# Kernel optimization log

Measured on AMD Instinct MI355X. Metric: run time of the kernel, lower is better.

Reference implementation:

```python
import jax, jax.numpy as jnp
import numpy as np

B, N, M = 64, 1024, 1024
MAX_ITER = 10      # init default max_iter
EPS = 1e-4         # init default epsilon


def setup_inputs() -> dict:
    key = jax.random.key(0)
    k1, k2, k3 = jax.random.split(key, 3)
    s = jax.random.uniform(k1, (B, N, M), dtype=jnp.float32)
    # ragged valid sizes per batch element, in [N//2, N]
    nrows = jax.random.randint(k2, (B,), N // 2, N + 1, dtype=jnp.int32)
    ncols = jax.random.randint(k3, (B,), M // 2, M + 1, dtype=jnp.int32)
    return {"s": s, "nrows": nrows, "ncols": ncols}


def reference(s, nrows, ncols):
    # Faithful vectorized form of the torch loop:
    #   even iter: sum[b,i,j] = sum_{k<nrows[b]} s[b,k,j]  (masked column sums)
    #   odd  iter: sum[b,i,j] = sum_{k<ncols[b]} s[b,i,k]  (masked row sums)
    #   then s[b,i,j] *= 1/sum inside the [nrows[b], ncols[b]] block, 0 outside.
    Bb, Nn, Mm = s.shape
    row_mask = jnp.arange(Nn)[None, :] < nrows[:, None]          # [B, N]
    col_mask = jnp.arange(Mm)[None, :] < ncols[:, None]          # [B, M]
    block = row_mask[:, :, None] & col_mask[:, None, :]          # [B, N, M]

    s = s + jnp.float32(EPS)
    for i in range(MAX_ITER):
        if i % 2 == 0:
            # column normalization: sum over valid rows
            d = jnp.sum(jnp.where(row_mask[:, :, None], s, 0.0), axis=1, keepdims=True)  # [B,1,M]
            d = jnp.where(col_mask[:, None, :], d, 1.0)  # safe denom outside block
        else:
            # row normalization: sum over valid cols
            d = jnp.sum(jnp.where(col_mask[:, None, :], s, 0.0), axis=2, keepdims=True)  # [B,N,1]
            d = jnp.where(row_mask[:, :, None], d, 1.0)
        s = jnp.where(block, s / d, 0.0)
    return s
```

## Files before the change

kernel.cpp:

```cpp
#include <hip/hip_runtime.h>


#define BB 64
#define NN 1024
#define MM 1024
#define EPS 1e-4f

typedef _Float16 half_t;
typedef __attribute__((ext_vector_type(4))) _Float16 half4_t;
typedef __attribute__((ext_vector_type(8))) _Float16 half8_t;
typedef __attribute__((ext_vector_type(4))) float float4_t;

__global__ __launch_bounds__(256) void prep_kernel(
    const float* __restrict__ s, const int* __restrict__ nrows,
    const int* __restrict__ ncols, half_t* __restrict__ H,
    float* __restrict__ P) {
  int b = blockIdx.z, rc = blockIdx.y, stripe = blockIdx.x;
  int nr = nrows[b], nc = ncols[b];
  float* Pp = P + ((size_t)rc * BB + b) * MM + stripe * 128;
  if (stripe * 128 >= nc) {
    if (threadIdx.x < 128) Pp[threadIdx.x] = 0.f;
    return;
  }
  int tc = threadIdx.x & 31, tr = threadIdx.x >> 5;
  int j0 = stripe * 128 + tc * 4;
  const float* sp = s + (size_t)b * NN * MM + j0;
  half_t* hp = H + (size_t)b * NN * MM + j0;
  float4_t acc = {0.f, 0.f, 0.f, 0.f};
  int base = rc * 128;
#pragma unroll
  for (int it = 0; it < 16; it++) {
    int i = base + it * 8 + tr;
    if (i < nr) {
      float4_t v = *(const float4_t*)(sp + (size_t)i * MM);
      v.x += EPS; v.y += EPS; v.z += EPS; v.w += EPS;
      half4_t h = {(half_t)v.x, (half_t)v.y, (half_t)v.z, (half_t)v.w};
      *(half4_t*)(hp + (size_t)i * MM) = h;
      acc.x += v.x; acc.y += v.y; acc.z += v.z; acc.w += v.w;
    }
  }
  __shared__ float lds[8][128];
  *(float4_t*)&lds[tr][tc * 4] = acc;
  __syncthreads();
  if (threadIdx.x < 128) {
    float s0 = 0.f;
#pragma unroll
    for (int k = 0; k < 8; k++) s0 += lds[k][threadIdx.x];
    Pp[threadIdx.x] = s0;
  }
}

__global__ __launch_bounds__(256) void creduce_kernel(
    const float* __restrict__ P, const int* __restrict__ ncols,
    float* __restrict__ C) {
  int b = blockIdx.y;
  int j = blockIdx.x * 256 + threadIdx.x;
  int nc = ncols[b];
  float s0 = 0.f;
#pragma unroll
  for (int k = 0; k < 8; k++) s0 += P[((size_t)k * BB + b) * MM + j];
  C[b * MM + j] = (j < nc) ? 1.f / s0 : 0.f;
}

__global__ __launch_bounds__(256) void row_kernel(
    const half_t* __restrict__ H, const int* __restrict__ nrows,
    const int* __restrict__ ncols, const float* __restrict__ C,
    float* __restrict__ R) {
  int b = blockIdx.y;
  int nr = nrows[b], nc = ncols[b];
  int w = threadIdx.x >> 6, l = threadIdx.x & 63;
  int i = blockIdx.x * 4 + w;
  if (i >= nr) return;
  const half_t* hp = H + ((size_t)b * NN + i) * MM;
  const float* Cp = C + b * MM;
  float acc = 0.f;
#pragma unroll
  for (int ch = 0; ch < 2; ch++) {
    int base = ch * 512 + l * 8;
    if (base < nc) {
      half8_t h = *(const half8_t*)(hp + base);
      float4_t c0 = *(const float4_t*)(Cp + base);
      float4_t c1 = *(const float4_t*)(Cp + base + 4);
      acc += (float)h[0] * c0.x + (float)h[1] * c0.y + (float)h[2] * c0.z +
             (float)h[3] * c0.w + (float)h[4] * c1.x + (float)h[5] * c1.y +
             (float)h[6] * c1.z + (float)h[7] * c1.w;
    }
  }
#pragma unroll
  for (int off = 32; off > 0; off >>= 1) acc += __shfl_xor(acc, off, 64);
  if (l == 0) R[b * NN + i] = 1.f / acc;
}

__global__ __launch_bounds__(256) void col_kernel(
    const half_t* __restrict__ H, const int* __restrict__ nrows,
    const int* __restrict__ ncols, const float* __restrict__ R,
    float* __restrict__ P) {
  int b = blockIdx.z, rc = blockIdx.y, stripe = blockIdx.x;
  int nr = nrows[b], nc = ncols[b];
  float* Pp = P + ((size_t)rc * BB + b) * MM + stripe * 256;
  if (stripe * 256 >= nc) {
    Pp[threadIdx.x] = 0.f;
    return;
  }
  int tc = threadIdx.x & 31, tr = threadIdx.x >> 5;
  int j0 = stripe * 256 + tc * 8;
  const half_t* hp = H + (size_t)b * NN * MM + j0;
  const float* Rp = R + b * NN;
  float acc[8] = {0.f, 0.f, 0.f, 0.f, 0.f, 0.f, 0.f, 0.f};
  int base = rc * 128;
#pragma unroll
  for (int it = 0; it < 16; it++) {
    int i = base + it * 8 + tr;
    if (i < nr) {
      half8_t h = *(const half8_t*)(hp + (size_t)i * MM);
      float r = Rp[i];
#pragma unroll
      for (int k = 0; k < 8; k++) acc[k] += (float)h[k] * r;
    }
  }
  __shared__ float lds[8][256];
#pragma unroll
  for (int k = 0; k < 8; k++) lds[tr][tc * 8 + k] = acc[k];
  __syncthreads();
  float s0 = 0.f;
#pragma unroll
  for (int k = 0; k < 8; k++) s0 += lds[k][threadIdx.x];
  Pp[threadIdx.x] = s0;
}

__global__ __launch_bounds__(256) void final_kernel(
    const float* __restrict__ s, const int* __restrict__ nrows,
    const int* __restrict__ ncols, const float* __restrict__ C,
    float* __restrict__ out) {
  int b = blockIdx.y;
  int nr = nrows[b], nc = ncols[b];
  int w = threadIdx.x >> 6, l = threadIdx.x & 63;
  int i = blockIdx.x * 4 + w;
  float* op = out + ((size_t)b * NN + i) * MM;
  float4_t z = {0.f, 0.f, 0.f, 0.f};
  if (i >= nr) {
#pragma unroll
    for (int ch = 0; ch < 4; ch++) *(float4_t*)(op + ch * 256 + l * 4) = z;
    return;
  }
  const float* sp = s + ((size_t)b * NN + i) * MM;
  const float* Cp = C + b * MM;
  float4_t sv[4], cv[4];
  float acc = 0.f;
  int nch = (nc + 255) >> 8;
#pragma unroll
  for (int ch = 0; ch < 4; ch++) {
    if (ch < nch) {
      float4_t v = *(const float4_t*)(sp + ch * 256 + l * 4);
      v.x += EPS; v.y += EPS; v.z += EPS; v.w += EPS;
      sv[ch] = v;
      float4_t c = *(const float4_t*)(Cp + ch * 256 + l * 4);
      cv[ch] = c;
      acc += v.x * c.x + v.y * c.y + v.z * c.z + v.w * c.w;
    }
  }
#pragma unroll
  for (int off = 32; off > 0; off >>= 1) acc += __shfl_xor(acc, off, 64);
  float r = 1.f / acc;
#pragma unroll
  for (int ch = 0; ch < 4; ch++) {
    if (ch < nch) {
      float4_t o;
      o.x = sv[ch].x * cv[ch].x * r;
      o.y = sv[ch].y * cv[ch].y * r;
      o.z = sv[ch].z * cv[ch].z * r;
      o.w = sv[ch].w * cv[ch].w * r;
      *(float4_t*)(op + ch * 256 + l * 4) = o;
    } else {
      *(float4_t*)(op + ch * 256 + l * 4) = z;
    }
  }
}

extern "C" void kernel_launch(void* const* d_in, const int* in_sizes, int n_in,
                              void* d_out, int out_size, void* d_ws,
                              size_t ws_size, hipStream_t stream) {
  const float* s = (const float*)d_in[0];
  const int* nrows = (const int*)d_in[1];
  const int* ncols = (const int*)d_in[2];
  float* out = (float*)d_out;
  half_t* H = (half_t*)d_out;
  float* R = (float*)d_ws;
  float* C = R + BB * NN;
  float* P = C + BB * MM;

  dim3 pgrid(8, 8, BB);
  dim3 cgrid(4, 8, BB);
  dim3 rgrid(NN / 4, BB);
  dim3 dgrid(4, BB);

  prep_kernel<<<pgrid, 256, 0, stream>>>(s, nrows, ncols, H, P);
  creduce_kernel<<<dgrid, 256, 0, stream>>>(P, ncols, C);
  for (int t = 0; t < 4; t++) {
    row_kernel<<<rgrid, 256, 0, stream>>>(H, nrows, ncols, C, R);
    col_kernel<<<cgrid, 256, 0, stream>>>(H, nrows, ncols, R, P);
    creduce_kernel<<<dgrid, 256, 0, stream>>>(P, ncols, C);
  }
  final_kernel<<<rgrid, 256, 0, stream>>>(s, nrows, ncols, C, out);
}
```

Baseline: 598.5 us.

## Fuse Sinkhorn iterations into one cooperative persistent kernel with fused row/col passes

Replaces the sequence of prep, row, column, reduce and final kernels with one cooperative kernel that uses grid-wide syncs between phases. The row-normalization dot product and the column partial sums now happen in a single pass over each half-precision row, so each iteration reads H once instead of twice and R no longer goes to memory. This removes about fifteen kernel launches and halves the intermediate traffic. In exchange it adds grid.sync costs, limits the grid to resident blocks, and uses a serial per-row loop with a wave reduction on every row.

After: 1.283 ms. 2.14x slower.

```diff
diff --git a/kernel.cpp b/kernel.cpp
--- a/kernel.cpp
+++ b/kernel.cpp
@@ -1,178 +1,190 @@
 #include <hip/hip_runtime.h>
+#include <hip/hip_cooperative_groups.h>
+
+namespace cg = cooperative_groups;
 
 
 #define BB 64
 #define NN 1024
 #define MM 1024
 #define EPS 1e-4f
+#define NCHUNK 16
+#define NITEM (BB * NCHUNK)
 
 typedef _Float16 half_t;
 typedef __attribute__((ext_vector_type(4))) _Float16 half4_t;
-typedef __attribute__((ext_vector_type(8))) _Float16 half8_t;
 typedef __attribute__((ext_vector_type(4))) float float4_t;
 
-__global__ __launch_bounds__(256) void prep_kernel(
+__device__ __forceinline__ float wave_sum(float v) {
+#pragma unroll
+  for (int off = 32; off > 0; off >>= 1) v += __shfl_xor(v, off, 64);
+  return v;
+}
+
+__global__ __launch_bounds__(256, 4) void sinkhorn_coop(
     const float* __restrict__ s, const int* __restrict__ nrows,
     const int* __restrict__ ncols, half_t* __restrict__ H,
-    float* __restrict__ P) {
-  int b = blockIdx.z, rc = blockIdx.y, stripe = blockIdx.x;
-  int nr = nrows[b], nc = ncols[b];
-  float* Pp = P + ((size_t)rc * BB + b) * MM + stripe * 128;
-  if (stripe * 128 >= nc) {
-    if (threadIdx.x < 128) Pp[threadIdx.x] = 0.f;
-    return;
+    float* __restrict__ C, float* __restrict__ P, float* __restrict__ out) {
+  cg::grid_group grid = cg::this_grid();
+  __shared__ float lds[4][MM];
+  const int tid = threadIdx.x;
+  const int w = tid >> 6, l = tid & 63;
+
+  for (int item = blockIdx.x; item < NITEM; item += gridDim.x) {
+    int b = item >> 4, chunk = item & 15;
+    int nr = nrows[b], nc = ncols[b];
+    int rbase = chunk * 64 + w * 16;
+    const float* sp = s + (size_t)b * NN * MM;
+    half_t* hp = H + (size_t)b * NN * MM;
+    float4_t ca[4];
+#pragma unroll
+    for (int c = 0; c < 4; c++) ca[c] = (float4_t){0.f, 0.f, 0.f, 0.f};
+    int nhere = min(nr - rbase, 16);
+    for (int rr = 0; rr < nhere; rr++) {
+      size_t roff = (size_t)(rbase + rr) * MM;
+#pragma unroll
+      for (int c = 0; c < 4; c++) {
+        if (c * 256 < nc) {
+          float4_t v = *(const float4_t*)(sp + roff + c * 256 + l * 4);
+          v.x += EPS; v.y += EPS; v.z += EPS; v.w += EPS;
+          half4_t h = {(half_t)v.x, (half_t)v.y, (half_t)v.z, (half_t)v.w};
+          *(half4_t*)(hp + roff + c * 256 + l * 4) = h;
+          ca[c].x += v.x; ca[c].y += v.y; ca[c].z += v.z; ca[c].w += v.w;
+        }
+      }
+    }
+    __syncthreads();
+#pragma unroll
+    for (int c = 0; c < 4; c++) *(float4_t*)&lds[w][c * 256 + l * 4] = ca[c];
+    __syncthreads();
+    {
+      float4_t a0 = *(float4_t*)&lds[0][tid * 4];
+      float4_t a1 = *(float4_t*)&lds[1][tid * 4];
+      float4_t a2 = *(float4_t*)&lds[2][tid * 4];
+      float4_t a3 = *(float4_t*)&lds[3][tid * 4];
+      float4_t r;
+      r.x = a0.x + a1.x + a2.x + a3.x;
+      r.y = a0.y + a1.y + a2.y + a3.y;
+      r.z = a0.z + a1.z + a2.z + a3.z;
+      r.w = a0.w + a1.w + a2.w + a3.w;
+      *(float4_t*)(P + (size_t)(chunk * BB + b) * MM + tid * 4) = r;
+    }
+    __syncthreads();
   }
-  int tc = threadIdx.x & 31, tr = threadIdx.x >> 5;
-  int j0 = stripe * 128 + tc * 4;
-  const float* sp = s + (size_t)b * NN * MM + j0;
-  half_t* hp = H + (size_t)b * NN * MM + j0;
-  float4_t acc = {0.f, 0.f, 0.f, 0.f};
-  int base = rc * 128;
-#pragma unroll
-  for (int it = 0; it < 16; it++) {
-    int i = base + it * 8 + tr;
-    if (i < nr) {
-      float4_t v = *(const float4_t*)(sp + (size_t)i * MM);
-      v.x += EPS; v.y += EPS; v.z += EPS; v.w += EPS;
-      half4_t h = {(half_t)v.x, (half_t)v.y, (half_t)v.z, (half_t)v.w};
-      *(half4_t*)(hp + (size_t)i * MM) = h;
-      acc.x += v.x; acc.y += v.y; acc.z += v.z; acc.w += v.w;
-    }
+  grid.sync();
+
+  for (int t = 0; t < 5; t++) {
+    for (int idx = blockIdx.x * 256 + tid; idx < BB * MM;
+         idx += gridDim.x * 256) {
+      int b = idx >> 10, j = idx & 1023;
+      float s0 = 0.f;
+#pragma unroll
+      for (int c = 0; c < NCHUNK; c++) s0 += P[(size_t)(c * BB + b) * MM + j];
+      C[idx] = (j < ncols[b]) ? 1.f / s0 : 0.f;
+    }
+    grid.sync();
+    if (t == 4) break;
+
+    for (int item = blockIdx.x; item < NITEM; item += gridDim.x) {
+      int b = item >> 4, chunk = item & 15;
+      int nr = nrows[b], nc = ncols[b];
+      const float* Cb = C + b * MM;
+      float4_t cv[4];
+#pragma unroll
+      for (int c = 0; c < 4; c++)
+        cv[c] = *(const float4_t*)(Cb + c * 256 + l * 4);
+      float4_t ca[4];
+#pragma unroll
+      for (int c = 0; c < 4; c++) ca[c] = (float4_t){0.f, 0.f, 0.f, 0.f};
+      const half_t* hp = H + (size_t)b * NN * MM;
+      int rbase = chunk * 64 + w * 16;
+      int nhere = min(nr - rbase, 16);
+      for (int rr = 0; rr < nhere; rr++) {
+        size_t roff = (size_t)(rbase + rr) * MM;
+        float4_t f[4];
+        float dot = 0.f;
+#pragma unroll
+        for (int c = 0; c < 4; c++) {
+          if (c * 256 < nc) {
+            half4_t h = *(const half4_t*)(hp + roff + c * 256 + l * 4);
+            f[c].x = (float)h[0]; f[c].y = (float)h[1];
+            f[c].z = (float)h[2]; f[c].w = (float)h[3];
+            dot += f[c].x * cv[c].x + f[c].y * cv[c].y + f[c].z * cv[c].z +
+                   f[c].w * cv[c].w;
+          }
+        }
+        float r = 1.f / wave_sum(dot);
+#pragma unroll
+        for (int c = 0; c < 4; c++) {
+          if (c * 256 < nc) {
+            ca[c].x += f[c].x * r; ca[c].y += f[c].y * r;
+            ca[c].z += f[c].z * r; ca[c].w += f[c].w * r;
+          }
+        }
+      }
+      __syncthreads();
+#pragma unroll
+      for (int c = 0; c < 4; c++) *(float4_t*)&lds[w][c * 256 + l * 4] = ca[c];
+      __syncthreads();
+      {
+        float4_t a0 = *(float4_t*)&lds[0][tid * 4];
+        float4_t a1 = *(float4_t*)&lds[1][tid * 4];
+        float4_t a2 = *(float4_t*)&lds[2][tid * 4];
+        float4_t a3 = *(float4_t*)&lds[3][tid * 4];
+        float4_t r;
+        r.x = a0.x + a1.x + a2.x + a3.x;
+        r.y = a0.y + a1.y + a2.y + a3.y;
+        r.z = a0.z + a1.z + a2.z + a3.z;
+        r.w = a0.w + a1.w + a2.w + a3.w;
+        *(float4_t*)(P + (size_t)(chunk * BB + b) * MM + tid * 4) = r;
+      }
+      __syncthreads();
+    }
+    grid.sync();
   }
-  __shared__ float lds[8][128];
-  *(float4_t*)&lds[tr][tc * 4] = acc;
-  __syncthreads();
-  if (threadIdx.x < 128) {
-    float s0 = 0.f;
-#pragma unroll
-    for (int k = 0; k < 8; k++) s0 += lds[k][threadIdx.x];
-    Pp[threadIdx.x] = s0;
-  }
-}
-
-__global__ __launch_bounds__(256) void creduce_kernel(
-    const float* __restrict__ P, const int* __restrict__ ncols,
-    float* __restrict__ C) {
-  int b = blockIdx.y;
-  int j = blockIdx.x * 256 + threadIdx.x;
-  int nc = ncols[b];
-  float s0 = 0.f;
-#pragma unroll
-  for (int k = 0; k < 8; k++) s0 += P[((size_t)k * BB + b) * MM + j];
-  C[b * MM + j] = (j < nc) ? 1.f / s0 : 0.f;
-}
-
-__global__ __launch_bounds__(256) void row_kernel(
-    const half_t* __restrict__ H, const int* __restrict__ nrows,
-    const int* __restrict__ ncols, const float* __restrict__ C,
-    float* __restrict__ R) {
-  int b = blockIdx.y;
-  int nr = nrows[b], nc = ncols[b];
-  int w = threadIdx.x >> 6, l = threadIdx.x & 63;
-  int i = blockIdx.x * 4 + w;
-  if (i >= nr) return;
-  const half_t* hp = H + ((size_t)b * NN + i) * MM;
-  const float* Cp = C + b * MM;
-  float acc = 0.f;
-#pragma unroll
-  for (int ch = 0; ch < 2; ch++) {
-    int base = ch * 512 + l * 8;
-    if (base < nc) {
-      half8_t h = *(const half8_t*)(hp + base);
-      float4_t c0 = *(const float4_t*)(Cp + base);
-      float4_t c1 = *(const float4_t*)(Cp + base + 4);
-      acc += (float)h[0] * c0.x + (float)h[1] * c0.y + (float)h[2] * c0.z +
-             (float)h[3] * c0.w + (float)h[4] * c1.x + (float)h[5] * c1.y +
-             (float)h[6] * c1.z + (float)h[7] * c1.w;
-    }
-  }
-#pragma unroll
-  for (int off = 32; off > 0; off >>= 1) acc += __shfl_xor(acc, off, 64);
-  if (l == 0) R[b * NN + i] = 1.f / acc;
-}
-
-__global__ __launch_bounds__(256) void col_kernel(
-    const half_t* __restrict__ H, const int* __restrict__ nrows,
-    const int* __restrict__ ncols, const float* __restrict__ R,
-    float* __restrict__ P) {
-  int b = blockIdx.z, rc = blockIdx.y, stripe = blockIdx.x;
-  int nr = nrows[b], nc = ncols[b];
-  float* Pp = P + ((size_t)rc * BB + b) * MM + stripe * 256;
-  if (stripe * 256 >= nc) {
-    Pp[threadIdx.x] = 0.f;
-    return;
-  }
-  int tc = threadIdx.x & 31, tr = threadIdx.x >> 5;
-  int j0 = stripe * 256 + tc * 8;
-  const half_t* hp = H + (size_t)b * NN * MM + j0;
-  const float* Rp = R + b * NN;
-  float acc[8] = {0.f, 0.f, 0.f, 0.f, 0.f, 0.f, 0.f, 0.f};
-  int base = rc * 128;
-#pragma unroll
-  for (int it = 0; it < 16; it++) {
-    int i = base + it * 8 + tr;
-    if (i < nr) {
-      half8_t h = *(const half8_t*)(hp + (size_t)i * MM);
-      float r = Rp[i];
-#pragma unroll
-      for (int k = 0; k < 8; k++) acc[k] += (float)h[k] * r;
-    }
-  }
-  __shared__ float lds[8][256];
-#pragma unroll
-  for (int k = 0; k < 8; k++) lds[tr][tc * 8 + k] = acc[k];
-  __syncthreads();
-  float s0 = 0.f;
-#pragma unroll
-  for (int k = 0; k < 8; k++) s0 += lds[k][threadIdx.x];
-  Pp[threadIdx.x] = s0;
-}
-
-__global__ __launch_bounds__(256) void final_kernel(
-    const float* __restrict__ s, const int* __restrict__ nrows,
-    const int* __restrict__ ncols, const float* __restrict__ C,
-    float* __restrict__ out) {
-  int b = blockIdx.y;
-  int nr = nrows[b], nc = ncols[b];
-  int w = threadIdx.x >> 6, l = threadIdx.x & 63;
-  int i = blockIdx.x * 4 + w;
-  float* op = out + ((size_t)b * NN + i) * MM;
-  float4_t z = {0.f, 0.f, 0.f, 0.f};
-  if (i >= nr) {
-#pragma unroll
-    for (int ch = 0; ch < 4; ch++) *(float4_t*)(op + ch * 256 + l * 4) = z;
-    return;
-  }
-  const float* sp = s + ((size_t)b * NN + i) * MM;
-  const float* Cp = C + b * MM;
-  float4_t sv[4], cv[4];
-  float acc = 0.f;
-  int nch = (nc + 255) >> 8;
-#pragma unroll
-  for (int ch = 0; ch < 4; ch++) {
-    if (ch < nch) {
-      float4_t v = *(const float4_t*)(sp + ch * 256 + l * 4);
-      v.x += EPS; v.y += EPS; v.z += EPS; v.w += EPS;
-      sv[ch] = v;
-      float4_t c = *(const float4_t*)(Cp + ch * 256 + l * 4);
-      cv[ch] = c;
-      acc += v.x * c.x + v.y * c.y + v.z * c.z + v.w * c.w;
-    }
-  }
-#pragma unroll
-  for (int off = 32; off > 0; off >>= 1) acc += __shfl_xor(acc, off, 64);
-  float r = 1.f / acc;
-#pragma unroll
-  for (int ch = 0; ch < 4; ch++) {
-    if (ch < nch) {
-      float4_t o;
-      o.x = sv[ch].x * cv[ch].x * r;
-      o.y = sv[ch].y * cv[ch].y * r;
-      o.z = sv[ch].z * cv[ch].z * r;
-      o.w = sv[ch].w * cv[ch].w * r;
-      *(float4_t*)(op + ch * 256 + l * 4) = o;
-    } else {
-      *(float4_t*)(op + ch * 256 + l * 4) = z;
+
+  for (int item = blockIdx.x; item < NITEM; item += gridDim.x) {
+    int b = item >> 4, chunk = item & 15;
+    int nr = nrows[b], nc = ncols[b];
+    const float* Cb = C + b * MM;
+    float4_t cv[4];
+#pragma unroll
+    for (int c = 0; c < 4; c++) cv[c] = *(const float4_t*)(Cb + c * 256 + l * 4);
+    int rbase = chunk * 64 + w * 16;
+    const float* sp = s + (size_t)b * NN * MM;
+    float* op = out + (size_t)b * NN * MM;
+    float4_t z = {0.f, 0.f, 0.f, 0.f};
+    for (int rr = 0; rr < 16; rr++) {
+      int i = rbase + rr;
+      size_t roff = (size_t)i * MM;
+      if (i < nr) {
+        float4_t f[4];
+        float dot = 0.f;
+#pragma unroll
+        for (int c = 0; c < 4; c++) {
+          if (c * 256 < nc) {
+            float4_t v = *(const float4_t*)(sp + roff + c * 256 + l * 4);
+            v.x += EPS; v.y += EPS; v.z += EPS; v.w += EPS;
+            f[c] = v;
+            dot += v.x * cv[c].x + v.y * cv[c].y + v.z * cv[c].z +
+                   v.w * cv[c].w;
+          }
+        }
+        float r = 1.f / wave_sum(dot);
+#pragma unroll
+        for (int c = 0; c < 4; c++) {
+          float4_t o = z;
+          if (c * 256 < nc) {
+            o.x = f[c].x * cv[c].x * r; o.y = f[c].y * cv[c].y * r;
+            o.z = f[c].z * cv[c].z * r; o.w = f[c].w * cv[c].w * r;
+          }
+          *(float4_t*)(op + roff + c * 256 + l * 4) = o;
+        }
+      } else {
+#pragma unroll
+        for (int c = 0; c < 4; c++)
+          *(float4_t*)(op + roff + c * 256 + l * 4) = z;
+      }
     }
   }
 }
@@ -185,21 +197,18 @@
   const int* ncols = (const int*)d_in[2];
   float* out = (float*)d_out;
   half_t* H = (half_t*)d_out;
-  float* R = (float*)d_ws;
-  float* C = R + BB * NN;
+  float* C = (float*)d_ws;
   float* P = C + BB * MM;
 
-  dim3 pgrid(8, 8, BB);
-  dim3 cgrid(4, 8, BB);
-  dim3 rgrid(NN / 4, BB);
-  dim3 dgrid(4, BB);
-
-  prep_kernel<<<pgrid, 256, 0, stream>>>(s, nrows, ncols, H, P);
-  creduce_kernel<<<dgrid, 256, 0, stream>>>(P, ncols, C);
-  for (int t = 0; t < 4; t++) {
-    row_kernel<<<rgrid, 256, 0, stream>>>(H, nrows, ncols, C, R);
-    col_kernel<<<cgrid, 256, 0, stream>>>(H, nrows, ncols, R, P);
-    creduce_kernel<<<dgrid, 256, 0, stream>>>(P, ncols, C);
-  }
-  final_kernel<<<rgrid, 256, 0, stream>>>(s, nrows, ncols, C, out);
+  int blocksPerCU = 0;
+  hipOccupancyMaxActiveBlocksPerMultiprocessor(&blocksPerCU, sinkhorn_coop,
+                                               256, 0);
+  if (blocksPerCU < 1) blocksPerCU = 1;
+  int G = blocksPerCU * 256;
+  if (G > NITEM) G = NITEM;
+
+  void* args[] = {(void*)&s, (void*)&nrows, (void*)&ncols,
+                  (void*)&H, (void*)&C,     (void*)&P,     (void*)&out};
+  hipLaunchCooperativeKernel(sinkhorn_coop, dim3(G), dim3(256), args, 0,
+                             stream);
 }
```
